# Performance work log

Hardware: AMD Instinct MI355X
Metric: run time of the kernel (lower is better)

The kernel has to match this reference:

```python
import jax, jax.numpy as jnp
import numpy as np


def setup_inputs() -> dict:
    key = jax.random.key(0)
    k1, k2, k3 = jax.random.split(key, 3)
    G, E, C, H, I = 1, 8, 2048, 1024, 4096
    x = jax.random.normal(k1, (G, E, C, H), dtype=jnp.float32)
    # init per module.reset_parameters: normal std sqrt(0.1/hidden) and sqrt(0.1/intermediate)
    wi = jax.random.normal(k2, (E, H, I), dtype=jnp.float32) * np.sqrt(0.1 / H)
    wo = jax.random.normal(k3, (E, I, H), dtype=jnp.float32) * np.sqrt(0.1 / I)
    return {"x": x, "wi": wi, "wo": wo}


def reference(x, wi, wo):
    # x: [G, E, C, H] -> transpose to [E, G, C, H] -> [E, G*C, H]
    G, E, C, H = x.shape
    xt = jnp.swapaxes(x, 0, 1).reshape(E, G * C, H)
    # per-expert grouped GEMM: hidden -> intermediate, gelu, -> hidden
    h = jax.nn.gelu(jnp.einsum("eth,ehi->eti", xt, wi), approximate=False)
    out = jnp.einsum("eti,eih->eth", h, wo)
    out = out.reshape(E, G, C, H)
    return jnp.swapaxes(out, 0, 1)  # [G, E, C, H]
```

## Files before the change

kernel.cpp:

```cpp
#include <hip/hip_runtime.h>
#include <hip/hip_bf16.h>
#include <cstdint>

typedef __attribute__((ext_vector_type(4))) float f32x4;
typedef __attribute__((ext_vector_type(8))) short bf16x8;
typedef __attribute__((ext_vector_type(4))) short s16x4;
typedef __attribute__((ext_vector_type(8))) short s16x8;

__device__ __forceinline__ short f2bf(float f) {
    union { float f; unsigned u; } v; v.f = f;
    unsigned r = v.u + 0x7FFFu + ((v.u >> 16) & 1u);
    return (short)(r >> 16);
}

__global__ __launch_bounds__(256) void cast_bf16(const float* __restrict__ in,
                                                 short* __restrict__ out, long n) {
    long i = ((long)blockIdx.x * 256 + threadIdx.x) * 8;
    if (i + 7 < n) {
        float4 a = *(const float4*)(in + i);
        float4 b = *(const float4*)(in + i + 4);
        s16x8 o;
        o[0] = f2bf(a.x); o[1] = f2bf(a.y); o[2] = f2bf(a.z); o[3] = f2bf(a.w);
        o[4] = f2bf(b.x); o[5] = f2bf(b.y); o[6] = f2bf(b.z); o[7] = f2bf(b.w);
        *(s16x8*)(out + i) = o;
    }
}

__global__ __launch_bounds__(256) void transpose_cast(const float* __restrict__ in,
                                                      short* __restrict__ out,
                                                      int R, int C) {
    __shared__ float t[64][65];
    const size_t eoff = (size_t)blockIdx.z * R * C;
    in  += eoff;
    out += eoff;
    const int c0 = blockIdx.x * 64, r0 = blockIdx.y * 64;
    const int tid = threadIdx.x;
    const int rr  = tid >> 4;
    const int cc4 = (tid & 15) * 4;
    #pragma unroll
    for (int i = 0; i < 4; ++i) {
        const int row = i * 16 + rr;
        float4 v = *(const float4*)(in + (size_t)(r0 + row) * C + c0 + cc4);
        t[row][cc4 + 0] = v.x; t[row][cc4 + 1] = v.y;
        t[row][cc4 + 2] = v.z; t[row][cc4 + 3] = v.w;
    }
    __syncthreads();
    #pragma unroll
    for (int i = 0; i < 4; ++i) {
        const int oc = i * 16 + rr;
        s16x4 o;
        o[0] = f2bf(t[cc4 + 0][oc]);
        o[1] = f2bf(t[cc4 + 1][oc]);
        o[2] = f2bf(t[cc4 + 2][oc]);
        o[3] = f2bf(t[cc4 + 3][oc]);
        *(s16x4*)(out + (size_t)(c0 + oc) * R + r0 + cc4) = o;
    }
}


#define FENCE() asm volatile("" ::: "memory")
#define BARRIER() do { FENCE(); __builtin_amdgcn_s_barrier(); FENCE(); } while (0)

__device__ __forceinline__ void stage2(const short* g0, const short* g1, short* l0) {
    __builtin_amdgcn_global_load_lds(
        (const __attribute__((address_space(1))) void*)g0,
        (__attribute__((address_space(3))) void*)l0, 16, 0, 0);
    __builtin_amdgcn_global_load_lds(
        (const __attribute__((address_space(1))) void*)g1,
        (__attribute__((address_space(3))) void*)(l0 + 4096), 16, 0, 0);
}

template <int FUSE>
__global__ __launch_bounds__(512, 2) void gemm_bt(const short* __restrict__ A,
                                                  const short* __restrict__ Bt,
                                                  void* __restrict__ Cout,
                                                  int M, int N, int K) {
    __shared__ short lds[65536];
    const int tid  = threadIdx.x;
    const int lane = tid & 63;
    const int wave = tid >> 6;
    const int wm   = wave >> 2;
    const int wn   = wave & 3;

    const int tilesM = M >> 8;
    const int perE   = tilesM * (N >> 8);
    const int total  = gridDim.x * gridDim.z;
    int lin = blockIdx.z * gridDim.x + blockIdx.x;
    lin = (lin & 7) * (total >> 3) + (lin >> 3);
    const int e   = lin / perE;
    const int rem = lin - e * perE;
    const int m0  = (rem % tilesM) << 8;
    const int n0  = (rem / tilesM) << 8;

    const short* Ab = A  + (size_t)e * M * K + (size_t)m0 * K;
    const short* Bb = Bt + (size_t)e * N * K + (size_t)n0 * K;

    size_t goff[2];
    #pragma unroll
    for (int i = 0; i < 2; ++i) {
        const int p  = i * 512 + tid;
        const int r  = p >> 2;
        const int sp = p & 3;
        const int q  = sp ^ ((r >> 1) & 3);
        goff[i] = (size_t)r * K + q * 8;
    }
    const int lwb = wave * 512;

    const int lrow = lane & 15, lq = lane >> 4;
    int offA[8], offB[4];
    #pragma unroll
    for (int m = 0; m < 8; ++m) {
        const int r = wm * 128 + m * 16 + lrow;
        offA[m] = (r * 4 + (lq ^ ((r >> 1) & 3))) * 8;
    }
    #pragma unroll
    for (int n = 0; n < 4; ++n) {
        const int r = wn * 64 + n * 16 + lrow;
        offB[n] = (r * 4 + (lq ^ ((r >> 1) & 3))) * 8;
    }

    f32x4 acc[8][4] = {};
    const int nk = K >> 5;

    #pragma unroll
    for (int t = 0; t < 3; ++t) {
        const size_t k0 = (size_t)t * 32;
        short* da = lds + (t & 3) * 8192 + lwb;
        short* db = lds + 32768 + (t & 3) * 8192 + lwb;
        stage2(Ab + k0 + goff[0], Ab + k0 + goff[1], da);
        stage2(Bb + k0 + goff[0], Bb + k0 + goff[1], db);
    }
    asm volatile("s_waitcnt vmcnt(8)" ::: "memory");
    BARRIER();

    for (int t = 0; t < nk; ++t) {
        const short* As = lds + (t & 3) * 8192;
        const short* Bs = lds + 32768 + (t & 3) * 8192;
        bf16x8 a0[4], b0[4], a1[4];

        #pragma unroll
        for (int m = 0; m < 4; ++m) a0[m] = *(const bf16x8*)(As + offA[m]);
        #pragma unroll
        for (int n = 0; n < 4; ++n) b0[n] = *(const bf16x8*)(Bs + offB[n]);
        if (t + 3 < nk) {
            const size_t k0 = (size_t)(t + 3) * 32;
            stage2(Ab + k0 + goff[0], Ab + k0 + goff[1],
                   lds + ((t + 3) & 3) * 8192 + lwb);
        }
        BARRIER();
        __builtin_amdgcn_s_setprio(1);
        #pragma unroll
        for (int m = 0; m < 4; ++m)
            #pragma unroll
            for (int n = 0; n < 4; ++n)
                acc[m][n] = __builtin_amdgcn_mfma_f32_16x16x32_bf16(
                    a0[m], b0[n], acc[m][n], 0, 0, 0);
        __builtin_amdgcn_s_setprio(0);
        BARRIER();

        #pragma unroll
        for (int m = 0; m < 4; ++m) a1[m] = *(const bf16x8*)(As + offA[4 + m]);
        if (t + 3 < nk) {
            const size_t k0 = (size_t)(t + 3) * 32;
            stage2(Bb + k0 + goff[0], Bb + k0 + goff[1],
                   lds + 32768 + ((t + 3) & 3) * 8192 + lwb);
        }
        if (t < nk - 3)       asm volatile("s_waitcnt vmcnt(8)" ::: "memory");
        else if (t == nk - 3) asm volatile("s_waitcnt vmcnt(4)" ::: "memory");
        else if (t == nk - 2) asm volatile("s_waitcnt vmcnt(0)" ::: "memory");
        BARRIER();
        __builtin_amdgcn_s_setprio(1);
        #pragma unroll
        for (int m = 0; m < 4; ++m)
            #pragma unroll
            for (int n = 0; n < 4; ++n)
                acc[4 + m][n] = __builtin_amdgcn_mfma_f32_16x16x32_bf16(
                    a1[m], b0[n], acc[4 + m][n], 0, 0, 0);
        __builtin_amdgcn_s_setprio(0);
        BARRIER();
    }

    const int r0q = lq << 2;
    const int cL  = lane & 15;
    if (FUSE) {
        short* C = (short*)Cout + (size_t)e * M * N;
        #pragma unroll
        for (int m = 0; m < 8; ++m)
            #pragma unroll
            for (int n = 0; n < 4; ++n)
                #pragma unroll
                for (int rr = 0; rr < 4; ++rr) {
                    const int row = m0 + wm * 128 + m * 16 + r0q + rr;
                    const int col = n0 + wn * 64 + n * 16 + cL;
                    float v = acc[m][n][rr];
                    v = 0.5f * v * (1.0f + erff(v * 0.70710678118654752f));
                    C[(size_t)row * N + col] = f2bf(v);
                }
    } else {
        float* C = (float*)Cout + (size_t)e * M * N;
        #pragma unroll
        for (int m = 0; m < 8; ++m)
            #pragma unroll
            for (int n = 0; n < 4; ++n)
                #pragma unroll
                for (int rr = 0; rr < 4; ++rr) {
                    const int row = m0 + wm * 128 + m * 16 + r0q + rr;
                    const int col = n0 + wn * 64 + n * 16 + cL;
                    C[(size_t)row * N + col] = acc[m][n][rr];
                }
    }
}

extern "C" void kernel_launch(void* const* d_in, const int* in_sizes, int n_in,
                              void* d_out, int out_size, void* d_ws, size_t ws_size,
                              hipStream_t stream) {
    constexpr int E = 8, Ct = 2048, H = 1024, I = 4096;

    const float* x  = (const float*)d_in[0];
    const float* wi = (const float*)d_in[1];
    const float* wo = (const float*)d_in[2];
    float* out = (float*)d_out;

    char* ws = (char*)d_ws;
    short* xb  = (short*)(ws);
    short* wiT = (short*)(ws + (size_t)33554432);
    short* woT = (short*)(ws + (size_t)100663296);
    short* h   = (short*)(ws + (size_t)167772160);

    {
        long n = (long)E * Ct * H;
        cast_bf16<<<dim3((unsigned)(n / 2048)), dim3(256), 0, stream>>>(x, xb, n);
    }
    transpose_cast<<<dim3(I / 64, H / 64, E), dim3(256), 0, stream>>>(wi, wiT, H, I);
    transpose_cast<<<dim3(H / 64, I / 64, E), dim3(256), 0, stream>>>(wo, woT, I, H);

    gemm_bt<1><<<dim3(128, 1, E), dim3(512), 0, stream>>>(xb, wiT, (void*)h, Ct, I, H);

    gemm_bt<0><<<dim3(32, 1, E), dim3(512), 0, stream>>>(h, woT, (void*)out, Ct, H, I);
}
```

Baseline: 636.3 us.

## Restructure GEMM main loop to BK=64 double-buffered halves with quadrant MFMA schedule

Switches the bf16 grouped GEMM K-step from 32 to 64 with a two-slot LDS double buffer split into A/B halves of 128 rows, replacing the four-slot ring of 32-wide tiles. The loop now runs four MFMA quadrant phases per iteration and interleaves half-tile global-to-LDS loads between them, using a new 8-way XOR swizzle on 64-wide rows. The aim is fewer barriers and waitcnts per unit of K, more MFMAs between synchronisations, and better LDS bank behaviour. The trade-offs are a shallower prefetch depth (one tile ahead instead of three) and more register pressure from holding fragments for two K sub-steps.

```diff
diff --git a/kernel.cpp b/kernel.cpp
--- a/kernel.cpp
+++ b/kernel.cpp
@@ -61,13 +61,14 @@
 #define FENCE() asm volatile("" ::: "memory")
 #define BARRIER() do { FENCE(); __builtin_amdgcn_s_barrier(); FENCE(); } while (0)
 
-__device__ __forceinline__ void stage2(const short* g0, const short* g1, short* l0) {
+__device__ __forceinline__ void stage_half(const short* __restrict__ g,
+                                           short* l, const size_t* goff) {
     __builtin_amdgcn_global_load_lds(
-        (const __attribute__((address_space(1))) void*)g0,
-        (__attribute__((address_space(3))) void*)l0, 16, 0, 0);
+        (const __attribute__((address_space(1))) void*)(g + goff[0]),
+        (__attribute__((address_space(3))) void*)l, 16, 0, 0);
     __builtin_amdgcn_global_load_lds(
-        (const __attribute__((address_space(1))) void*)g1,
-        (__attribute__((address_space(3))) void*)(l0 + 4096), 16, 0, 0);
+        (const __attribute__((address_space(1))) void*)(g + goff[1]),
+        (__attribute__((address_space(3))) void*)(l + 4096), 16, 0, 0);
 }
 
 template <int FUSE>
@@ -94,15 +95,15 @@
 
     const short* Ab = A  + (size_t)e * M * K + (size_t)m0 * K;
     const short* Bb = Bt + (size_t)e * N * K + (size_t)n0 * K;
+    const size_t hK = (size_t)128 * K;
 
     size_t goff[2];
     #pragma unroll
     for (int i = 0; i < 2; ++i) {
         const int p  = i * 512 + tid;
-        const int r  = p >> 2;
-        const int sp = p & 3;
-        const int q  = sp ^ ((r >> 1) & 3);
-        goff[i] = (size_t)r * K + q * 8;
+        const int r  = p >> 3;
+        const int sp = p & 7;
+        goff[i] = (size_t)r * K + (size_t)((sp ^ (r & 7)) << 3);
     }
     const int lwb = wave * 512;
 
@@ -110,72 +111,127 @@
     int offA[8], offB[4];
     #pragma unroll
     for (int m = 0; m < 8; ++m) {
-        const int r = wm * 128 + m * 16 + lrow;
-        offA[m] = (r * 4 + (lq ^ ((r >> 1) & 3))) * 8;
+        const int rh = m * 16 + lrow;
+        offA[m] = wm * 8192 + rh * 64 + ((lq ^ (rh & 7)) << 3);
     }
     #pragma unroll
     for (int n = 0; n < 4; ++n) {
-        const int r = wn * 64 + n * 16 + lrow;
-        offB[n] = (r * 4 + (lq ^ ((r >> 1) & 3))) * 8;
+        const int row = wn * 64 + n * 16 + lrow;
+        const int h = row >> 7, rh = row & 127;
+        offB[n] = 16384 + h * 8192 + rh * 64 + ((lq ^ (rh & 7)) << 3);
     }
 
     f32x4 acc[8][4] = {};
-    const int nk = K >> 5;
-
-    #pragma unroll
-    for (int t = 0; t < 3; ++t) {
-        const size_t k0 = (size_t)t * 32;
-        short* da = lds + (t & 3) * 8192 + lwb;
-        short* db = lds + 32768 + (t & 3) * 8192 + lwb;
-        stage2(Ab + k0 + goff[0], Ab + k0 + goff[1], da);
-        stage2(Bb + k0 + goff[0], Bb + k0 + goff[1], db);
-    }
-    asm volatile("s_waitcnt vmcnt(8)" ::: "memory");
+    const int nk = K >> 6;
+
+    stage_half(Ab,      lds +     0 + lwb, goff);
+    stage_half(Ab + hK, lds +  8192 + lwb, goff);
+    stage_half(Bb,      lds + 16384 + lwb, goff);
+    stage_half(Bb + hK, lds + 24576 + lwb, goff);
+    if (nk > 1) {
+        const short* A1p = Ab + 64;
+        const short* B1p = Bb + 64;
+        stage_half(B1p,      lds + 32768 + 16384 + lwb, goff);
+        stage_half(B1p + hK, lds + 32768 + 24576 + lwb, goff);
+        stage_half(A1p,      lds + 32768 +     0 + lwb, goff);
+        asm volatile("s_waitcnt vmcnt(6)" ::: "memory");
+    } else {
+        asm volatile("s_waitcnt vmcnt(0)" ::: "memory");
+    }
     BARRIER();
 
+    bf16x8 Af[4][2], Bf0[2][2], Bf1[2][2];
+
     for (int t = 0; t < nk; ++t) {
-        const short* As = lds + (t & 3) * 8192;
-        const short* Bs = lds + 32768 + (t & 3) * 8192;
-        bf16x8 a0[4], b0[4], a1[4];
-
-        #pragma unroll
-        for (int m = 0; m < 4; ++m) a0[m] = *(const bf16x8*)(As + offA[m]);
-        #pragma unroll
-        for (int n = 0; n < 4; ++n) b0[n] = *(const bf16x8*)(Bs + offB[n]);
-        if (t + 3 < nk) {
-            const size_t k0 = (size_t)(t + 3) * 32;
-            stage2(Ab + k0 + goff[0], Ab + k0 + goff[1],
-                   lds + ((t + 3) & 3) * 8192 + lwb);
-        }
-        BARRIER();
-        __builtin_amdgcn_s_setprio(1);
-        #pragma unroll
-        for (int m = 0; m < 4; ++m)
-            #pragma unroll
-            for (int n = 0; n < 4; ++n)
-                acc[m][n] = __builtin_amdgcn_mfma_f32_16x16x32_bf16(
-                    a0[m], b0[n], acc[m][n], 0, 0, 0);
-        __builtin_amdgcn_s_setprio(0);
-        BARRIER();
-
-        #pragma unroll
-        for (int m = 0; m < 4; ++m) a1[m] = *(const bf16x8*)(As + offA[4 + m]);
-        if (t + 3 < nk) {
-            const size_t k0 = (size_t)(t + 3) * 32;
-            stage2(Bb + k0 + goff[0], Bb + k0 + goff[1],
-                   lds + 32768 + ((t + 3) & 3) * 8192 + lwb);
-        }
-        if (t < nk - 3)       asm volatile("s_waitcnt vmcnt(8)" ::: "memory");
-        else if (t == nk - 3) asm volatile("s_waitcnt vmcnt(4)" ::: "memory");
-        else if (t == nk - 2) asm volatile("s_waitcnt vmcnt(0)" ::: "memory");
-        BARRIER();
-        __builtin_amdgcn_s_setprio(1);
-        #pragma unroll
-        for (int m = 0; m < 4; ++m)
-            #pragma unroll
-            for (int n = 0; n < 4; ++n)
-                acc[4 + m][n] = __builtin_amdgcn_mfma_f32_16x16x32_bf16(
-                    a1[m], b0[n], acc[4 + m][n], 0, 0, 0);
+        const int sl  = (t & 1) << 15;
+        const int slN = ((t + 1) & 1) << 15;
+        const short* S = lds + sl;
+        const short* An1 = Ab + (size_t)(t + 1) * 64;
+        const short* An2 = Ab + (size_t)(t + 2) * 64;
+        const short* Bn2 = Bb + (size_t)(t + 2) * 64;
+
+        #pragma unroll
+        for (int i = 0; i < 4; ++i) {
+            const int o = offA[i];
+            Af[i][0] = *(const bf16x8*)(S + o);
+            Af[i][1] = *(const bf16x8*)(S + (o ^ 32));
+        }
+        #pragma unroll
+        for (int j = 0; j < 2; ++j) {
+            const int o = offB[j];
+            Bf0[j][0] = *(const bf16x8*)(S + o);
+            Bf0[j][1] = *(const bf16x8*)(S + (o ^ 32));
+        }
+        if (t + 1 < nk) stage_half(An1 + hK, lds + slN + 8192 + lwb, goff);
+        BARRIER();
+        __builtin_amdgcn_s_setprio(1);
+        #pragma unroll
+        for (int s = 0; s < 2; ++s)
+            #pragma unroll
+            for (int i = 0; i < 4; ++i)
+                #pragma unroll
+                for (int j = 0; j < 2; ++j)
+                    acc[i][j] = __builtin_amdgcn_mfma_f32_16x16x32_bf16(
+                        Af[i][s], Bf0[j][s], acc[i][j], 0, 0, 0);
+        __builtin_amdgcn_s_setprio(0);
+        BARRIER();
+
+        #pragma unroll
+        for (int j = 0; j < 2; ++j) {
+            const int o = offB[2 + j];
+            Bf1[j][0] = *(const bf16x8*)(S + o);
+            Bf1[j][1] = *(const bf16x8*)(S + (o ^ 32));
+        }
+        BARRIER();
+        __builtin_amdgcn_s_setprio(1);
+        #pragma unroll
+        for (int s = 0; s < 2; ++s)
+            #pragma unroll
+            for (int i = 0; i < 4; ++i)
+                #pragma unroll
+                for (int j = 0; j < 2; ++j)
+                    acc[i][2 + j] = __builtin_amdgcn_mfma_f32_16x16x32_bf16(
+                        Af[i][s], Bf1[j][s], acc[i][2 + j], 0, 0, 0);
+        __builtin_amdgcn_s_setprio(0);
+        BARRIER();
+
+        #pragma unroll
+        for (int i = 0; i < 4; ++i) {
+            const int o = offA[4 + i];
+            Af[i][0] = *(const bf16x8*)(S + o);
+            Af[i][1] = *(const bf16x8*)(S + (o ^ 32));
+        }
+        if (t + 2 < nk) stage_half(Bn2, lds + sl + 16384 + lwb, goff);
+        BARRIER();
+        __builtin_amdgcn_s_setprio(1);
+        #pragma unroll
+        for (int s = 0; s < 2; ++s)
+            #pragma unroll
+            for (int i = 0; i < 4; ++i)
+                #pragma unroll
+                for (int j = 0; j < 2; ++j)
+                    acc[4 + i][2 + j] = __builtin_amdgcn_mfma_f32_16x16x32_bf16(
+                        Af[i][s], Bf1[j][s], acc[4 + i][2 + j], 0, 0, 0);
+        __builtin_amdgcn_s_setprio(0);
+        BARRIER();
+
+        if (t + 2 < nk) {
+            stage_half(Bn2 + hK, lds + sl + 24576 + lwb, goff);
+            stage_half(An2,      lds + sl +     0 + lwb, goff);
+            asm volatile("s_waitcnt vmcnt(6)" ::: "memory");
+        } else {
+            asm volatile("s_waitcnt vmcnt(0)" ::: "memory");
+        }
+        BARRIER();
+        __builtin_amdgcn_s_setprio(1);
+        #pragma unroll
+        for (int s = 0; s < 2; ++s)
+            #pragma unroll
+            for (int i = 0; i < 4; ++i)
+                #pragma unroll
+                for (int j = 0; j < 2; ++j)
+                    acc[4 + i][j] = __builtin_amdgcn_mfma_f32_16x16x32_bf16(
+                        Af[i][s], Bf0[j][s], acc[4 + i][j], 0, 0, 0);
         __builtin_amdgcn_s_setprio(0);
         BARRIER();
     }
```

Result: faster. 614.3 us (-3.5%).
